# Kernel tuning notes

Measured on AMD Instinct MI355X. Metric: run time of the kernel, lower is better.

## Reference

```python
import jax, jax.numpy as jnp
import numpy as np

HEADS = 8
DIM_HEAD = 64
INNER = HEADS * DIM_HEAD  # 512
QUERY_DIM = 1024
CONTEXT_DIM = 768
OUT_DIM = 1024


def setup_inputs() -> dict:
    key = jax.random.key(0)
    ks = jax.random.split(key, 7)
    B, Nq, Nk = 2, 4096, 4096
    s = 0.02
    return {
        "x": jax.random.normal(ks[0], (B, Nq, QUERY_DIM), dtype=jnp.float32),
        "context": jax.random.normal(ks[1], (B, Nk, CONTEXT_DIM), dtype=jnp.float32),
        "w_q": jax.random.normal(ks[2], (QUERY_DIM, INNER), dtype=jnp.float32) * s,
        "w_k": jax.random.normal(ks[3], (CONTEXT_DIM, INNER), dtype=jnp.float32) * s,
        "w_v": jax.random.normal(ks[4], (CONTEXT_DIM, INNER), dtype=jnp.float32) * s,
        "w_out": jax.random.normal(ks[5], (INNER, OUT_DIM), dtype=jnp.float32) * s,
        "b_out": jax.random.normal(ks[6], (OUT_DIM,), dtype=jnp.float32) * s,
    }


def reference(x, context, w_q, w_k, w_v, w_out, b_out):
    h, d = HEADS, DIM_HEAD
    scale = d ** (-0.5)
    B, Nq, _ = x.shape
    Nk = context.shape[1]
    # projections (no bias)
    q = x @ w_q            # [B, Nq, h*d]
    k = context @ w_k      # [B, Nk, h*d]
    v = context @ w_v      # [B, Nk, h*d]
    # split heads: b n (h d) -> b h n d
    q = q.reshape(B, Nq, h, d).transpose(0, 2, 1, 3)
    k = k.reshape(B, Nk, h, d).transpose(0, 2, 1, 3)
    v = v.reshape(B, Nk, h, d).transpose(0, 2, 1, 3)
    sim = jnp.einsum('bhid,bhjd->bhij', q, k) * scale  # [B, h, Nq, Nk]
    attn = jax.nn.softmax(sim, axis=-1)
    out = jnp.einsum('bhij,bhjd->bhid', attn, v)       # [B, h, Nq, d]
    out = out.transpose(0, 2, 1, 3).reshape(B, Nq, h * d)
    return out @ w_out + b_out  # dropout p=0 -> identity
```

## Files before the change

kernel.cpp:

```cpp
#include <hip/hip_runtime.h>
#include <hip/hip_bf16.h>
#include <stdint.h>

#define HEADS 8
#define DHEAD 64
#define INNER 512
#define QDIM 1024
#define CDIM 768
#define ODIM 1024
#define BATCH 2
#define NQ 4096
#define NKEY 4096

using bf16x8 = __attribute__((ext_vector_type(8))) short;
using f32x4  = __attribute__((ext_vector_type(4))) float;

__device__ __forceinline__ unsigned short f2bf(float x) {
    union { float f; unsigned u; } v; v.f = x;
    unsigned r = v.u + 0x7fffu + ((v.u >> 16) & 1u);
    return (unsigned short)(r >> 16);
}

__device__ __forceinline__ unsigned cvtpk(float a, float b) {
    unsigned r;
    asm("v_cvt_pk_bf16_f32 %0, %1, %2" : "=v"(r) : "v"(a), "v"(b));
    return r;
}

__device__ __forceinline__ float exp2a(float x) {
    float r;
    asm("v_exp_f32 %0, %1" : "=v"(r) : "v"(x));
    return r;
}

typedef const __attribute__((address_space(1))) unsigned int* gptr_t;
typedef __attribute__((address_space(3))) unsigned int* lptr_t;

__device__ __forceinline__ void async16(const void* g, void* l) {
    __builtin_amdgcn_global_load_lds((gptr_t)g, (lptr_t)l, 16, 0, 0);
}

__global__ void k_convert(const float* __restrict__ in, unsigned short* __restrict__ out, int n4) {
    int i = blockIdx.x * blockDim.x + threadIdx.x;
    int stride = gridDim.x * blockDim.x;
    for (; i < n4; i += stride) {
        float4 v = reinterpret_cast<const float4*>(in)[i];
        ushort4 o;
        o.x = f2bf(v.x); o.y = f2bf(v.y); o.z = f2bf(v.z); o.w = f2bf(v.w);
        reinterpret_cast<ushort4*>(out)[i] = o;
    }
}

__global__ void k_transpose_bf16(const float* __restrict__ in, unsigned short* __restrict__ out,
                                 int R, int C) {
    __shared__ float tile[32][33];
    int c0 = blockIdx.x * 32, r0 = blockIdx.y * 32;
    int tx = threadIdx.x, ty = threadIdx.y;
    #pragma unroll
    for (int i = 0; i < 32; i += 8)
        tile[ty + i][tx] = in[(size_t)(r0 + ty + i) * C + c0 + tx];
    __syncthreads();
    #pragma unroll
    for (int i = 0; i < 32; i += 8)
        out[(size_t)(c0 + ty + i) * R + r0 + tx] = f2bf(tile[tx][ty + i]);
}

template <int OUTMODE>
__global__ __launch_bounds__(256) void k_gemm(const unsigned short* __restrict__ A,
                                              const unsigned short* __restrict__ BT,
                                              void* __restrict__ Cout,
                                              const float* __restrict__ bias,
                                              int M, int N, int Kd, float scale) {
    __shared__ alignas(16) unsigned short As[128 * 64];
    __shared__ alignas(16) unsigned short Bs[64 * 64];
    const int tid = threadIdx.x, lane = tid & 63, w = tid >> 6;
    const int g = lane >> 4, ql = lane & 15;
    const int m0 = blockIdx.x * 128, n0 = blockIdx.y * 64;
    const int wm = (w >> 1) * 64, wn = (w & 1) * 32;
    f32x4 acc[4][2] = {};

    const int srow = tid >> 3;
    const int schunk = ((tid & 7) ^ (srow & 7)) << 3;
    const unsigned short* gA = A + (size_t)(m0 + srow) * Kd + schunk;
    const unsigned short* gB = BT + (size_t)(n0 + srow) * Kd + schunk;
    char* lA = (char*)As + (w << 10);
    char* lB = (char*)Bs + (w << 10);

    for (int kt = 0; kt < Kd; kt += 64) {
        __syncthreads();
        async16(gA + kt, lA);
        async16(gA + kt + (size_t)32 * Kd, lA + 4096);
        async16(gA + kt + (size_t)64 * Kd, lA + 8192);
        async16(gA + kt + (size_t)96 * Kd, lA + 12288);
        async16(gB + kt, lB);
        async16(gB + kt + (size_t)32 * Kd, lB + 4096);
        __syncthreads();

        #pragma unroll
        for (int kk = 0; kk < 2; kk++) {
            bf16x8 af[4], bfr[2];
            #pragma unroll
            for (int mi = 0; mi < 4; mi++) {
                int r = wm + mi * 16 + ql;
                af[mi] = *(const bf16x8*)((const char*)As + r * 128 + ((kk * 64 + (g << 4)) ^ ((r & 7) << 4)));
            }
            #pragma unroll
            for (int ni = 0; ni < 2; ni++) {
                int r = wn + ni * 16 + ql;
                bfr[ni] = *(const bf16x8*)((const char*)Bs + r * 128 + ((kk * 64 + (g << 4)) ^ ((r & 7) << 4)));
            }
            #pragma unroll
            for (int mi = 0; mi < 4; mi++)
                #pragma unroll
                for (int ni = 0; ni < 2; ni++)
                    acc[mi][ni] = __builtin_amdgcn_mfma_f32_16x16x32_bf16(af[mi], bfr[ni], acc[mi][ni], 0, 0, 0);
        }
    }

    #pragma unroll
    for (int mi = 0; mi < 4; mi++) {
        #pragma unroll
        for (int ni = 0; ni < 2; ni++) {
            int col = n0 + wn + ni * 16 + ql;
            #pragma unroll
            for (int j = 0; j < 4; j++) {
                int row = m0 + wm + mi * 16 + (g << 2) + j;
                float v = acc[mi][ni][j] * scale;
                if (OUTMODE == 0) {
                    ((unsigned short*)Cout)[(size_t)row * N + col] = f2bf(v);
                } else {
                    ((float*)Cout)[(size_t)row * N + col] = v + bias[col];
                }
            }
        }
    }
}

__global__ __launch_bounds__(256, 2) void k_attn(const unsigned short* __restrict__ Q,
                                                 const unsigned short* __restrict__ K,
                                                 const unsigned short* __restrict__ Vt,
                                                 unsigned short* __restrict__ O) {
    __shared__ alignas(16) unsigned short Ks[2][64 * 64];
    __shared__ alignas(16) unsigned short Vs[2][64 * 64];
    const int tid = threadIdx.x, lane = tid & 63, w = tid >> 6;
    const int g = lane >> 4, ql = lane & 15;
    const int q0 = blockIdx.x * 128;
    const int b = blockIdx.y >> 3, h = blockIdx.y & 7;

    const unsigned short* qp = Q + (size_t)(b * NQ + q0 + w * 32 + ql) * INNER
                                 + h * DHEAD + (g << 3);
    bf16x8 qf00 = *(const bf16x8*)qp;
    bf16x8 qf01 = *(const bf16x8*)(qp + 32);
    bf16x8 qf10 = *(const bf16x8*)(qp + 16 * INNER);
    bf16x8 qf11 = *(const bf16x8*)(qp + 16 * INNER + 32);

    f32x4 po0[4] = {}, po1[4] = {};
    float ls0 = 0.f, ls1 = 0.f;
    const f32x4 zero4 = {0.f, 0.f, 0.f, 0.f};

    const int m0 = tid >> 3;
    const int rho0 = ((m0 & 28) << 1) + (m0 & 3);
    const int srcslot = ((tid & 7) ^ (m0 & 7)) << 3;
    const unsigned short* gK = K + (size_t)(b * NKEY + rho0) * INNER + h * DHEAD + srcslot;
    const unsigned short* gV = Vt + (size_t)(h * DHEAD + m0) * (BATCH * NKEY) + b * NKEY + srcslot;

    auto stageK = [&](int nb, int kt) {
        char* lK = (char*)Ks[nb] + (w << 10);
        async16(gK + (size_t)kt * INNER, lK);
        async16(gK + (size_t)(kt + 4) * INNER, lK + 4096);
    };
    auto stageV = [&](int nb, int kt) {
        char* lV = (char*)Vs[nb] + (w << 10);
        async16(gV + kt, lV);
        async16(gV + kt + (size_t)32 * (BATCH * NKEY), lV + 4096);
    };

    union pfu { bf16x8 v; unsigned u[4]; };

#define QKM(KBUF, S0, S1) { \
        const char* Kb_ = (const char*)(KBUF); \
        _Pragma("unroll") \
        for (int mi = 0; mi < 4; mi++) { \
            int rK = mi * 16 + ql; \
            int sw = (rK & 7) << 4; \
            bf16x8 kf0 = *(const bf16x8*)(Kb_ + rK * 128 + ((g << 4) ^ sw)); \
            bf16x8 kf1 = *(const bf16x8*)(Kb_ + rK * 128 + ((64 + (g << 4)) ^ sw)); \
            S0[mi] = __builtin_amdgcn_mfma_f32_16x16x32_bf16(kf0, qf00, zero4, 0, 0, 0); \
            S0[mi] = __builtin_amdgcn_mfma_f32_16x16x32_bf16(kf1, qf01, S0[mi], 0, 0, 0); \
            S1[mi] = __builtin_amdgcn_mfma_f32_16x16x32_bf16(kf0, qf10, zero4, 0, 0, 0); \
            S1[mi] = __builtin_amdgcn_mfma_f32_16x16x32_bf16(kf1, qf11, S1[mi], 0, 0, 0); \
        } \
    }

#define SMCHUNK(MI, SC0, SC1, pA, pB, lsa, lsb) { \
        float a0 = exp2a(SC0[MI][0]), a1 = exp2a(SC0[MI][1]); \
        float a2 = exp2a(SC0[MI][2]), a3 = exp2a(SC0[MI][3]); \
        float b0 = exp2a(SC1[MI][0]), b1 = exp2a(SC1[MI][1]); \
        float b2 = exp2a(SC1[MI][2]), b3 = exp2a(SC1[MI][3]); \
        lsa += (a0 + a1) + (a2 + a3); \
        lsb += (b0 + b1) + (b2 + b3); \
        pA[MI & 1].u[(MI >> 1) * 2 + 0] = cvtpk(a0, a1); \
        pA[MI & 1].u[(MI >> 1) * 2 + 1] = cvtpk(a2, a3); \
        pB[MI & 1].u[(MI >> 1) * 2 + 0] = cvtpk(b0, b1); \
        pB[MI & 1].u[(MI >> 1) * 2 + 1] = cvtpk(b2, b3); \
    }

#define PVM(VBUF, pA, pB) { \
        const char* Vb_ = (const char*)(VBUF); \
        bf16x8 vf0[4], vf1[4]; \
        _Pragma("unroll") \
        for (int mi = 0; mi < 4; mi++) { \
            int rV = mi * 16 + ql; \
            int sw = (rV & 7) << 4; \
            vf0[mi] = *(const bf16x8*)(Vb_ + rV * 128 + ((g << 4) ^ sw)); \
            vf1[mi] = *(const bf16x8*)(Vb_ + rV * 128 + ((64 + (g << 4)) ^ sw)); \
        } \
        _Pragma("unroll") \
        for (int mi = 0; mi < 4; mi++) { \
            po0[mi] = __builtin_amdgcn_mfma_f32_16x16x32_bf16(vf0[mi], pA[0].v, po0[mi], 0, 0, 0); \
            po0[mi] = __builtin_amdgcn_mfma_f32_16x16x32_bf16(vf1[mi], pA[1].v, po0[mi], 0, 0, 0); \
            po1[mi] = __builtin_amdgcn_mfma_f32_16x16x32_bf16(vf0[mi], pB[0].v, po1[mi], 0, 0, 0); \
            po1[mi] = __builtin_amdgcn_mfma_f32_16x16x32_bf16(vf1[mi], pB[1].v, po1[mi], 0, 0, 0); \
        } \
    }

#define BODY(T, CUR, SC0, SC1, SN0, SN1, DOSTAGEK) { \
        if (DOSTAGEK) stageK(CUR, (T + 2) * 64); \
        stageV(CUR ^ 1, (T + 1) * 64); \
        const char* Kb_ = (const char*)Ks[CUR ^ 1]; \
        bf16x8 kf0[4], kf1[4]; \
        _Pragma("unroll") \
        for (int mi = 0; mi < 4; mi++) { \
            int rK = mi * 16 + ql; \
            int sw = (rK & 7) << 4; \
            kf0[mi] = *(const bf16x8*)(Kb_ + rK * 128 + ((g << 4) ^ sw)); \
            kf1[mi] = *(const bf16x8*)(Kb_ + rK * 128 + ((64 + (g << 4)) ^ sw)); \
        } \
        __builtin_amdgcn_sched_group_barrier(0x100, 8, 0); \
        pfu pA[2], pB[2]; \
        float lsa = 0.f, lsb = 0.f; \
        _Pragma("unroll") \
        for (int mi = 0; mi < 4; mi++) { \
            SMCHUNK(mi, SC0, SC1, pA, pB, lsa, lsb); \
            __builtin_amdgcn_sched_group_barrier(0x2, 18, 0); \
            SN0[mi] = __builtin_amdgcn_mfma_f32_16x16x32_bf16(kf0[mi], qf00, zero4, 0, 0, 0); \
            SN0[mi] = __builtin_amdgcn_mfma_f32_16x16x32_bf16(kf1[mi], qf01, SN0[mi], 0, 0, 0); \
            SN1[mi] = __builtin_amdgcn_mfma_f32_16x16x32_bf16(kf0[mi], qf10, zero4, 0, 0, 0); \
            SN1[mi] = __builtin_amdgcn_mfma_f32_16x16x32_bf16(kf1[mi], qf11, SN1[mi], 0, 0, 0); \
            __builtin_amdgcn_sched_group_barrier(0x8, 4, 0); \
        } \
        ls0 += lsa; ls1 += lsb; \
        __builtin_amdgcn_s_setprio(1); \
        PVM(Vs[CUR], pA, pB); \
        __builtin_amdgcn_sched_group_barrier(0x100, 8, 0); \
        __builtin_amdgcn_sched_group_barrier(0x8, 16, 0); \
        __builtin_amdgcn_s_setprio(0); \
        __syncthreads(); \
    }

    f32x4 sE0[4], sE1[4], sO0[4], sO1[4];

    stageK(0, 0); stageV(0, 0); stageK(1, 64);
    __syncthreads();
    QKM(Ks[0], sE0, sE1);
    __syncthreads();

    for (int t = 0; t < 62; t += 2) {
        BODY(t, 0, sE0, sE1, sO0, sO1, 1);
        BODY(t + 1, 1, sO0, sO1, sE0, sE1, 1);
    }
    BODY(62, 0, sE0, sE1, sO0, sO1, 0);
    {
        pfu pA[2], pB[2];
        float lsa = 0.f, lsb = 0.f;
        #pragma unroll
        for (int mi = 0; mi < 4; mi++) {
            SMCHUNK(mi, sO0, sO1, pA, pB, lsa, lsb);
        }
        ls0 += lsa; ls1 += lsb;
        PVM(Vs[1], pA, pB);
    }

    ls0 += __shfl_xor(ls0, 16); ls0 += __shfl_xor(ls0, 32);
    ls1 += __shfl_xor(ls1, 16); ls1 += __shfl_xor(ls1, 32);
    float inv0 = 1.0f / ls0, inv1 = 1.0f / ls1;
    unsigned short* op = O + (size_t)(b * NQ + q0 + w * 32 + ql) * INNER + h * DHEAD + (g << 2);
    #pragma unroll
    for (int mi = 0; mi < 4; mi++) {
        uint2 uu;
        uu.x = cvtpk(po0[mi][0] * inv0, po0[mi][1] * inv0);
        uu.y = cvtpk(po0[mi][2] * inv0, po0[mi][3] * inv0);
        *(uint2*)(op + mi * 16) = uu;
        uint2 vv;
        vv.x = cvtpk(po1[mi][0] * inv1, po1[mi][1] * inv1);
        vv.y = cvtpk(po1[mi][2] * inv1, po1[mi][3] * inv1);
        *(uint2*)(op + 16 * INNER + mi * 16) = vv;
    }
#undef BODY
#undef PVM
#undef SMCHUNK
#undef QKM
}

extern "C" void kernel_launch(void* const* d_in, const int* in_sizes, int n_in,
                              void* d_out, int out_size, void* d_ws, size_t ws_size,
                              hipStream_t stream) {
    const float* x     = (const float*)d_in[0];
    const float* ctx   = (const float*)d_in[1];
    const float* w_q   = (const float*)d_in[2];
    const float* w_k   = (const float*)d_in[3];
    const float* w_v   = (const float*)d_in[4];
    const float* w_out = (const float*)d_in[5];
    const float* b_out = (const float*)d_in[6];
    float* out = (float*)d_out;

    char* ws = (char*)d_ws;
    size_t off = 0;
    auto alloc = [&](size_t bytes) { void* p = ws + off; off += (bytes + 255) & ~(size_t)255; return p; };
    unsigned short* xb  = (unsigned short*)alloc((size_t)BATCH * NQ * QDIM * 2);
    unsigned short* cb  = (unsigned short*)alloc((size_t)BATCH * NKEY * CDIM * 2);
    unsigned short* wqT = (unsigned short*)alloc((size_t)INNER * QDIM * 2);
    unsigned short* wkT = (unsigned short*)alloc((size_t)INNER * CDIM * 2);
    unsigned short* wvT = (unsigned short*)alloc((size_t)INNER * CDIM * 2);
    unsigned short* woT = (unsigned short*)alloc((size_t)ODIM * INNER * 2);
    unsigned short* Qb  = (unsigned short*)alloc((size_t)BATCH * NQ * INNER * 2);
    unsigned short* Kb  = (unsigned short*)alloc((size_t)BATCH * NKEY * INNER * 2);
    unsigned short* Vtb = (unsigned short*)alloc((size_t)INNER * BATCH * NKEY * 2);
    unsigned short* Ob  = (unsigned short*)alloc((size_t)BATCH * NQ * INNER * 2);

    k_convert<<<2048, 256, 0, stream>>>(x, xb, BATCH * NQ * QDIM / 4);
    k_convert<<<2048, 256, 0, stream>>>(ctx, cb, BATCH * NKEY * CDIM / 4);

    dim3 tb(32, 8);
    k_transpose_bf16<<<dim3(INNER / 32, QDIM / 32), tb, 0, stream>>>(w_q, wqT, QDIM, INNER);
    k_transpose_bf16<<<dim3(INNER / 32, CDIM / 32), tb, 0, stream>>>(w_k, wkT, CDIM, INNER);
    k_transpose_bf16<<<dim3(INNER / 32, CDIM / 32), tb, 0, stream>>>(w_v, wvT, CDIM, INNER);
    k_transpose_bf16<<<dim3(ODIM / 32, INNER / 32), tb, 0, stream>>>(w_out, woT, INNER, ODIM);

    k_gemm<0><<<dim3(8192 / 128, 512 / 64), 256, 0, stream>>>(xb, wqT, Qb, nullptr, 8192, 512, 1024, 0.1803368801111204f);
    k_gemm<0><<<dim3(8192 / 128, 512 / 64), 256, 0, stream>>>(cb, wkT, Kb, nullptr, 8192, 512, 768, 1.0f);
    k_gemm<0><<<dim3(512 / 128, 8192 / 64), 256, 0, stream>>>(wvT, cb, Vtb, nullptr, 512, 8192, 768, 1.0f);

    k_attn<<<dim3(NQ / 128, BATCH * HEADS), 256, 0, stream>>>(Qb, Kb, Vtb, Ob);

    k_gemm<1><<<dim3(8192 / 128, 1024 / 64), 256, 0, stream>>>(Ob, woT, out, b_out, 8192, 1024, 512, 1.0f);
}
```

Before: 156.9 us.

## Double-buffer GEMM LDS tiles and restructure attention loop sync and scheduling

The projection GEMM now uses two LDS buffers, so the next K tile's async global-to-LDS loads are issued while the current tile is computed, with one barrier per tile instead of two. The attention loop body is reorganised to wait on vmcnt and barrier at the top of each iteration, then issue the next K/V staging and load the V fragments up front. Fine-grained sched_group_barriers interleave exp, MFMA and LDS reads. This aims to overlap memory latency with compute and cut barrier stalls, at the cost of doubled GEMM LDS use (lower occupancy) and more fragile hand-tuned scheduling.

```diff
diff --git a/kernel.cpp b/kernel.cpp
--- a/kernel.cpp
+++ b/kernel.cpp
@@ -39,6 +39,8 @@
 __device__ __forceinline__ void async16(const void* g, void* l) {
     __builtin_amdgcn_global_load_lds((gptr_t)g, (lptr_t)l, 16, 0, 0);
 }
+
+#define SGB __builtin_amdgcn_sched_group_barrier
 
 __global__ void k_convert(const float* __restrict__ in, unsigned short* __restrict__ out, int n4) {
     int i = blockIdx.x * blockDim.x + threadIdx.x;
@@ -71,8 +73,8 @@
                                               void* __restrict__ Cout,
                                               const float* __restrict__ bias,
                                               int M, int N, int Kd, float scale) {
-    __shared__ alignas(16) unsigned short As[128 * 64];
-    __shared__ alignas(16) unsigned short Bs[64 * 64];
+    __shared__ alignas(16) unsigned short As[2][128 * 64];
+    __shared__ alignas(16) unsigned short Bs[2][64 * 64];
     const int tid = threadIdx.x, lane = tid & 63, w = tid >> 6;
     const int g = lane >> 4, ql = lane & 15;
     const int m0 = blockIdx.x * 128, n0 = blockIdx.y * 64;
@@ -83,39 +85,54 @@
     const int schunk = ((tid & 7) ^ (srow & 7)) << 3;
     const unsigned short* gA = A + (size_t)(m0 + srow) * Kd + schunk;
     const unsigned short* gB = BT + (size_t)(n0 + srow) * Kd + schunk;
-    char* lA = (char*)As + (w << 10);
-    char* lB = (char*)Bs + (w << 10);
-
-    for (int kt = 0; kt < Kd; kt += 64) {
-        __syncthreads();
+
+    auto stage = [&](int buf, int kt) {
+        char* lA = (char*)As[buf] + (w << 10);
+        char* lB = (char*)Bs[buf] + (w << 10);
         async16(gA + kt, lA);
         async16(gA + kt + (size_t)32 * Kd, lA + 4096);
         async16(gA + kt + (size_t)64 * Kd, lA + 8192);
         async16(gA + kt + (size_t)96 * Kd, lA + 12288);
         async16(gB + kt, lB);
         async16(gB + kt + (size_t)32 * Kd, lB + 4096);
-        __syncthreads();
-
-        #pragma unroll
-        for (int kk = 0; kk < 2; kk++) {
-            bf16x8 af[4], bfr[2];
-            #pragma unroll
-            for (int mi = 0; mi < 4; mi++) {
-                int r = wm + mi * 16 + ql;
-                af[mi] = *(const bf16x8*)((const char*)As + r * 128 + ((kk * 64 + (g << 4)) ^ ((r & 7) << 4)));
-            }
-            #pragma unroll
-            for (int ni = 0; ni < 2; ni++) {
-                int r = wn + ni * 16 + ql;
-                bfr[ni] = *(const bf16x8*)((const char*)Bs + r * 128 + ((kk * 64 + (g << 4)) ^ ((r & 7) << 4)));
-            }
-            #pragma unroll
-            for (int mi = 0; mi < 4; mi++)
-                #pragma unroll
-                for (int ni = 0; ni < 2; ni++)
-                    acc[mi][ni] = __builtin_amdgcn_mfma_f32_16x16x32_bf16(af[mi], bfr[ni], acc[mi][ni], 0, 0, 0);
-        }
-    }
+    };
+
+#define GCOMP(BUF) { \
+        _Pragma("unroll") \
+        for (int kk = 0; kk < 2; kk++) { \
+            bf16x8 af[4], bfr[2]; \
+            _Pragma("unroll") \
+            for (int mi = 0; mi < 4; mi++) { \
+                int r = wm + mi * 16 + ql; \
+                af[mi] = *(const bf16x8*)((const char*)As[BUF] + r * 128 + ((kk * 64 + (g << 4)) ^ ((r & 7) << 4))); \
+            } \
+            _Pragma("unroll") \
+            for (int ni = 0; ni < 2; ni++) { \
+                int r = wn + ni * 16 + ql; \
+                bfr[ni] = *(const bf16x8*)((const char*)Bs[BUF] + r * 128 + ((kk * 64 + (g << 4)) ^ ((r & 7) << 4))); \
+            } \
+            _Pragma("unroll") \
+            for (int mi = 0; mi < 4; mi++) \
+                _Pragma("unroll") \
+                for (int ni = 0; ni < 2; ni++) \
+                    acc[mi][ni] = __builtin_amdgcn_mfma_f32_16x16x32_bf16(af[mi], bfr[ni], acc[mi][ni], 0, 0, 0); \
+        } \
+    }
+
+    stage(0, 0);
+    for (int kt = 0; kt < Kd; kt += 128) {
+        asm volatile("s_waitcnt vmcnt(0)" ::: "memory");
+        __builtin_amdgcn_s_barrier();
+        __builtin_amdgcn_sched_barrier(0);
+        if (kt + 64 < Kd) stage(1, kt + 64);
+        GCOMP(0);
+        asm volatile("s_waitcnt vmcnt(0)" ::: "memory");
+        __builtin_amdgcn_s_barrier();
+        __builtin_amdgcn_sched_barrier(0);
+        if (kt + 128 < Kd) stage(0, kt + 128);
+        GCOMP(1);
+    }
+#undef GCOMP
 
     #pragma unroll
     for (int mi = 0; mi < 4; mi++) {
@@ -177,21 +194,6 @@
 
     union pfu { bf16x8 v; unsigned u[4]; };
 
-#define QKM(KBUF, S0, S1) { \
-        const char* Kb_ = (const char*)(KBUF); \
-        _Pragma("unroll") \
-        for (int mi = 0; mi < 4; mi++) { \
-            int rK = mi * 16 + ql; \
-            int sw = (rK & 7) << 4; \
-            bf16x8 kf0 = *(const bf16x8*)(Kb_ + rK * 128 + ((g << 4) ^ sw)); \
-            bf16x8 kf1 = *(const bf16x8*)(Kb_ + rK * 128 + ((64 + (g << 4)) ^ sw)); \
-            S0[mi] = __builtin_amdgcn_mfma_f32_16x16x32_bf16(kf0, qf00, zero4, 0, 0, 0); \
-            S0[mi] = __builtin_amdgcn_mfma_f32_16x16x32_bf16(kf1, qf01, S0[mi], 0, 0, 0); \
-            S1[mi] = __builtin_amdgcn_mfma_f32_16x16x32_bf16(kf0, qf10, zero4, 0, 0, 0); \
-            S1[mi] = __builtin_amdgcn_mfma_f32_16x16x32_bf16(kf1, qf11, S1[mi], 0, 0, 0); \
-        } \
-    }
-
 #define SMCHUNK(MI, SC0, SC1, pA, pB, lsa, lsb) { \
         float a0 = exp2a(SC0[MI][0]), a1 = exp2a(SC0[MI][1]); \
         float a2 = exp2a(SC0[MI][2]), a3 = exp2a(SC0[MI][3]); \
@@ -205,9 +207,37 @@
         pB[MI & 1].u[(MI >> 1) * 2 + 1] = cvtpk(b2, b3); \
     }
 
-#define PVM(VBUF, pA, pB) { \
-        const char* Vb_ = (const char*)(VBUF); \
-        bf16x8 vf0[4], vf1[4]; \
+#define QKM(KBUF, S0, S1) { \
+        const char* Kb_ = (const char*)(KBUF); \
+        _Pragma("unroll") \
+        for (int mi = 0; mi < 4; mi++) { \
+            int rK = mi * 16 + ql; \
+            int sw = (rK & 7) << 4; \
+            bf16x8 kf0 = *(const bf16x8*)(Kb_ + rK * 128 + ((g << 4) ^ sw)); \
+            bf16x8 kf1 = *(const bf16x8*)(Kb_ + rK * 128 + ((64 + (g << 4)) ^ sw)); \
+            S0[mi] = __builtin_amdgcn_mfma_f32_16x16x32_bf16(kf0, qf00, zero4, 0, 0, 0); \
+            S0[mi] = __builtin_amdgcn_mfma_f32_16x16x32_bf16(kf1, qf01, S0[mi], 0, 0, 0); \
+            S1[mi] = __builtin_amdgcn_mfma_f32_16x16x32_bf16(kf0, qf10, zero4, 0, 0, 0); \
+            S1[mi] = __builtin_amdgcn_mfma_f32_16x16x32_bf16(kf1, qf11, S1[mi], 0, 0, 0); \
+        } \
+    }
+
+#define ABODY(T, CUR, SC0, SC1, SN0, SN1, DO_K, DO_V) { \
+        asm volatile("s_waitcnt vmcnt(0)" ::: "memory"); \
+        __builtin_amdgcn_s_barrier(); \
+        __builtin_amdgcn_sched_barrier(0); \
+        if (DO_K) stageK(CUR, (T + 2) * 64); \
+        if (DO_V) stageV(CUR ^ 1, (T + 1) * 64); \
+        const char* Kb_ = (const char*)Ks[CUR ^ 1]; \
+        const char* Vb_ = (const char*)Vs[CUR]; \
+        bf16x8 kf0[4], kf1[4], vf0[4], vf1[4]; \
+        _Pragma("unroll") \
+        for (int mi = 0; mi < 4; mi++) { \
+            int rK = mi * 16 + ql; \
+            int sw = (rK & 7) << 4; \
+            kf0[mi] = *(const bf16x8*)(Kb_ + rK * 128 + ((g << 4) ^ sw)); \
+            kf1[mi] = *(const bf16x8*)(Kb_ + rK * 128 + ((64 + (g << 4)) ^ sw)); \
+        } \
         _Pragma("unroll") \
         for (int mi = 0; mi < 4; mi++) { \
             int rV = mi * 16 + ql; \
@@ -215,6 +245,24 @@
             vf0[mi] = *(const bf16x8*)(Vb_ + rV * 128 + ((g << 4) ^ sw)); \
             vf1[mi] = *(const bf16x8*)(Vb_ + rV * 128 + ((64 + (g << 4)) ^ sw)); \
         } \
+        SGB(0x10, 4, 0);    \
+        pfu pA[2], pB[2]; \
+        float lsa = 0.f, lsb = 0.f; \
+        _Pragma("unroll") \
+        for (int mi = 0; mi < 4; mi++) { \
+            SMCHUNK(mi, SC0, SC1, pA, pB, lsa, lsb); \
+            SN0[mi] = __builtin_amdgcn_mfma_f32_16x16x32_bf16(kf0[mi], qf00, zero4, 0, 0, 0); \
+            SN0[mi] = __builtin_amdgcn_mfma_f32_16x16x32_bf16(kf1[mi], qf01, SN0[mi], 0, 0, 0); \
+            SN1[mi] = __builtin_amdgcn_mfma_f32_16x16x32_bf16(kf0[mi], qf10, zero4, 0, 0, 0); \
+            SN1[mi] = __builtin_amdgcn_mfma_f32_16x16x32_bf16(kf1[mi], qf11, SN1[mi], 0, 0, 0); \
+            SGB(0x100, 4, 0); \
+            SGB(0x8, 1, 0); SGB(0x400, 4, 0); SGB(0x2, 3, 0); \
+            SGB(0x8, 1, 0); SGB(0x400, 4, 0); SGB(0x2, 3, 0); \
+            SGB(0x8, 1, 0); SGB(0x400, 4, 0); SGB(0x2, 3, 0); \
+            SGB(0x8, 1, 0); SGB(0x400, 4, 0); SGB(0x2, 4, 0); \
+        } \
+        ls0 += lsa; ls1 += lsb; \
+        __builtin_amdgcn_s_setprio(1); \
         _Pragma("unroll") \
         for (int mi = 0; mi < 4; mi++) { \
             po0[mi] = __builtin_amdgcn_mfma_f32_16x16x32_bf16(vf0[mi], pA[0].v, po0[mi], 0, 0, 0); \
@@ -222,55 +270,36 @@
             po1[mi] = __builtin_amdgcn_mfma_f32_16x16x32_bf16(vf0[mi], pB[0].v, po1[mi], 0, 0, 0); \
             po1[mi] = __builtin_amdgcn_mfma_f32_16x16x32_bf16(vf1[mi], pB[1].v, po1[mi], 0, 0, 0); \
         } \
-    }
-
-#define BODY(T, CUR, SC0, SC1, SN0, SN1, DOSTAGEK) { \
-        if (DOSTAGEK) stageK(CUR, (T + 2) * 64); \
-        stageV(CUR ^ 1, (T + 1) * 64); \
-        const char* Kb_ = (const char*)Ks[CUR ^ 1]; \
-        bf16x8 kf0[4], kf1[4]; \
-        _Pragma("unroll") \
-        for (int mi = 0; mi < 4; mi++) { \
-            int rK = mi * 16 + ql; \
-            int sw = (rK & 7) << 4; \
-            kf0[mi] = *(const bf16x8*)(Kb_ + rK * 128 + ((g << 4) ^ sw)); \
-            kf1[mi] = *(const bf16x8*)(Kb_ + rK * 128 + ((64 + (g << 4)) ^ sw)); \
-        } \
-        __builtin_amdgcn_sched_group_barrier(0x100, 8, 0); \
-        pfu pA[2], pB[2]; \
-        float lsa = 0.f, lsb = 0.f; \
-        _Pragma("unroll") \
-        for (int mi = 0; mi < 4; mi++) { \
-            SMCHUNK(mi, SC0, SC1, pA, pB, lsa, lsb); \
-            __builtin_amdgcn_sched_group_barrier(0x2, 18, 0); \
-            SN0[mi] = __builtin_amdgcn_mfma_f32_16x16x32_bf16(kf0[mi], qf00, zero4, 0, 0, 0); \
-            SN0[mi] = __builtin_amdgcn_mfma_f32_16x16x32_bf16(kf1[mi], qf01, SN0[mi], 0, 0, 0); \
-            SN1[mi] = __builtin_amdgcn_mfma_f32_16x16x32_bf16(kf0[mi], qf10, zero4, 0, 0, 0); \
-            SN1[mi] = __builtin_amdgcn_mfma_f32_16x16x32_bf16(kf1[mi], qf11, SN1[mi], 0, 0, 0); \
-            __builtin_amdgcn_sched_group_barrier(0x8, 4, 0); \
-        } \
-        ls0 += lsa; ls1 += lsb; \
-        __builtin_amdgcn_s_setprio(1); \
-        PVM(Vs[CUR], pA, pB); \
-        __builtin_amdgcn_sched_group_barrier(0x100, 8, 0); \
-        __builtin_amdgcn_sched_group_barrier(0x8, 16, 0); \
         __builtin_amdgcn_s_setprio(0); \
-        __syncthreads(); \
     }
 
     f32x4 sE0[4], sE1[4], sO0[4], sO1[4];
 
     stageK(0, 0); stageV(0, 0); stageK(1, 64);
-    __syncthreads();
+    asm volatile("s_waitcnt vmcnt(2)" ::: "memory");
+    __builtin_amdgcn_s_barrier();
+    __builtin_amdgcn_sched_barrier(0);
     QKM(Ks[0], sE0, sE1);
-    __syncthreads();
 
     for (int t = 0; t < 62; t += 2) {
-        BODY(t, 0, sE0, sE1, sO0, sO1, 1);
-        BODY(t + 1, 1, sO0, sO1, sE0, sE1, 1);
-    }
-    BODY(62, 0, sE0, sE1, sO0, sO1, 0);
+        ABODY(t, 0, sE0, sE1, sO0, sO1, 1, 1);
+        ABODY(t + 1, 1, sO0, sO1, sE0, sE1, 1, 1);
+    }
+    ABODY(62, 0, sE0, sE1, sO0, sO1, 0, 1);
+
+    asm volatile("s_waitcnt vmcnt(0)" ::: "memory");
+    __builtin_amdgcn_s_barrier();
+    __builtin_amdgcn_sched_barrier(0);
     {
+        const char* Vb_ = (const char*)Vs[1];
+        bf16x8 vf0[4], vf1[4];
+        #pragma unroll
+        for (int mi = 0; mi < 4; mi++) {
+            int rV = mi * 16 + ql;
+            int sw = (rV & 7) << 4;
+            vf0[mi] = *(const bf16x8*)(Vb_ + rV * 128 + ((g << 4) ^ sw));
+            vf1[mi] = *(const bf16x8*)(Vb_ + rV * 128 + ((64 + (g << 4)) ^ sw));
+        }
         pfu pA[2], pB[2];
         float lsa = 0.f, lsb = 0.f;
         #pragma unroll
@@ -278,7 +307,13 @@
             SMCHUNK(mi, sO0, sO1, pA, pB, lsa, lsb);
         }
         ls0 += lsa; ls1 += lsb;
-        PVM(Vs[1], pA, pB);
+        #pragma unroll
+        for (int mi = 0; mi < 4; mi++) {
+            po0[mi] = __builtin_amdgcn_mfma_f32_16x16x32_bf16(vf0[mi], pA[0].v, po0[mi], 0, 0, 0);
+            po0[mi] = __builtin_amdgcn_mfma_f32_16x16x32_bf16(vf1[mi], pA[1].v, po0[mi], 0, 0, 0);
+            po1[mi] = __builtin_amdgcn_mfma_f32_16x16x32_bf16(vf0[mi], pB[0].v, po1[mi], 0, 0, 0);
+            po1[mi] = __builtin_amdgcn_mfma_f32_16x16x32_bf16(vf1[mi], pB[1].v, po1[mi], 0, 0, 0);
+        }
     }
 
     ls0 += __shfl_xor(ls0, 16); ls0 += __shfl_xor(ls0, 32);
@@ -296,10 +331,9 @@
         vv.y = cvtpk(po1[mi][2] * inv1, po1[mi][3] * inv1);
         *(uint2*)(op + 16 * INNER + mi * 16) = vv;
     }
-#undef BODY
-#undef PVM
+#undef ABODY
+#undef QKM
 #undef SMCHUNK
-#undef QKM
 }
 
 extern "C" void kernel_launch(void* const* d_in, const int* in_sizes, int n_in,
```

Measured after the change: 163.6 us. 1.04x slower.
